# Kernel tuning notes

Hardware: AMD Instinct MI355X
Metric: run time of the kernel (lower is better)

The kernel has to match this reference:

```python
import jax, jax.numpy as jnp
import numpy as np


def setup_inputs() -> dict:
    key = jax.random.key(0)
    k1, k2 = jax.random.split(key)
    B, S, K, N = 8, 2048, 2048, 2048
    a = jax.random.normal(k1, (B, S, K), dtype=jnp.float32)
    b = jax.random.normal(k2, (B, K, N), dtype=jnp.float32)
    return {"a": a, "b": b}


def reference(a, b):
    # Per-sample dense: out[i] = a[i] @ b[i], fused as one batched GEMM.
    # a: [B, S, K], b: [B, K, N] -> out: [B, S, N]
    return jnp.einsum('bsk,bkn->bsn', a, b)
```

## Files before the change

### kernel.cpp

```cpp
#include <hip/hip_runtime.h>

#define BATCH 8
#define SDIM 2048
#define KDIM 2048
#define NDIM 2048

typedef __bf16 bf16_t;
typedef bf16_t bf16x4 __attribute__((ext_vector_type(4)));
typedef bf16_t bf16x8 __attribute__((ext_vector_type(8)));
typedef float f32x4 __attribute__((ext_vector_type(4)));
typedef float f32x8 __attribute__((ext_vector_type(8)));
typedef unsigned short u16x8 __attribute__((ext_vector_type(8)));

__device__ __forceinline__ void gl_lds16(const void* g, void* l) {
    __builtin_amdgcn_global_load_lds(
        (__attribute__((address_space(1))) void*)g,
        (__attribute__((address_space(3))) void*)l,
        16, 0, 0);
}

__global__ __launch_bounds__(256)
void cvtA_kernel(const float* __restrict__ A, bf16_t* __restrict__ Abf) {
    const size_t total8 = (size_t)BATCH * SDIM * KDIM / 8;
    const size_t stride = (size_t)gridDim.x * 256;
    for (size_t i = (size_t)blockIdx.x * 256 + threadIdx.x; i < total8; i += stride) {
        f32x8 v = *reinterpret_cast<const f32x8*>(A + i * 8);
        *reinterpret_cast<bf16x8*>(Abf + i * 8) = __builtin_convertvector(v, bf16x8);
    }
}

__global__ __launch_bounds__(256)
void cvtBT_kernel(const float* __restrict__ B, bf16_t* __restrict__ Bt) {
    __shared__ alignas(16) bf16_t T[64][72];
    const int gid = blockIdx.x;
    const int batch = gid & 7;
    const int tile = gid >> 3;
    const int k0g = (tile >> 5) * 64;
    const int n0g = (tile & 31) * 64;
    const float* Bb = B + (size_t)batch * KDIM * NDIM + (size_t)k0g * NDIM + n0g;
    bf16_t* Tb = Bt + (size_t)batch * NDIM * KDIM + (size_t)n0g * KDIM + k0g;

    const int t = threadIdx.x;
    const int kq = t & 15;
    const int nq = t >> 4;
    f32x4 v[4];
#pragma unroll
    for (int r = 0; r < 4; ++r)
        v[r] = *reinterpret_cast<const f32x4*>(Bb + (size_t)(kq * 4 + r) * NDIM + nq * 4);
#pragma unroll
    for (int j = 0; j < 4; ++j) {
        bf16x4 w = {(bf16_t)v[0][j], (bf16_t)v[1][j], (bf16_t)v[2][j], (bf16_t)v[3][j]};
        *reinterpret_cast<bf16x4*>(&T[nq * 4 + j][kq * 4]) = w;
    }
    __syncthreads();
    const int n = t >> 2, kc = t & 3;
    bf16x8 o0 = *reinterpret_cast<const bf16x8*>(&T[n][kc * 16]);
    bf16x8 o1 = *reinterpret_cast<const bf16x8*>(&T[n][kc * 16 + 8]);
    *reinterpret_cast<bf16x8*>(Tb + (size_t)n * KDIM + kc * 16) = o0;
    *reinterpret_cast<bf16x8*>(Tb + (size_t)n * KDIM + kc * 16 + 8) = o1;
}

#define VM4 asm volatile("s_waitcnt vmcnt(4)" ::: "memory")
#define VM0 asm volatile("s_waitcnt vmcnt(0)" ::: "memory")
#define NOOP ((void)0)

__global__ __launch_bounds__(512, 2)
void bgemm_pipe(const bf16_t* __restrict__ A, const bf16_t* __restrict__ Bt,
                float* __restrict__ O) {
    __shared__ alignas(16) bf16_t lds[65536];

    const int tid = threadIdx.x;
    const int gid = blockIdx.x;
    const int batch = gid & 7;
    const int t = gid >> 3;
    const int bm = (t >> 3) * 256;
    const int bn = (t & 7) * 256;

    const int lane = tid & 63;
    const int wid = tid >> 6;
    const int wr = wid >> 2;
    const int wc = wid & 3;
    const int lr = lane & 15;
    const int lq = lane >> 4;

    const bf16_t* Ab = A + (size_t)batch * SDIM * KDIM;
    const bf16_t* Bb = Bt + (size_t)batch * NDIM * KDIM;
    float* Ob = O + (size_t)batch * SDIM * NDIM;

    const bf16_t* aSrc0 = Ab + (size_t)(bm + wid * 32 + lr) * KDIM + lq * 8;
    const bf16_t* aSrc1 = aSrc0 + (size_t)16 * KDIM;
    const bf16_t* bSrc0 = Bb + (size_t)(bn + wid * 32 + lr) * KDIM + lq * 8;
    const bf16_t* bSrc1 = bSrc0 + (size_t)16 * KDIM;

    const int aDst0 = (wid * 2) * 512;
    const int aDst1 = (wid * 2 + 1) * 512;
    const int rdA = lq * 128 + lr * 8;
    const int rdB = 8192 + lq * 128 + lr * 8;

#define STAGE(BUF_, KT_) do { \
    gl_lds16(aSrc0 + (size_t)(KT_) * 32, &lds[(BUF_) * 16384 + aDst0]); \
    gl_lds16(aSrc1 + (size_t)(KT_) * 32, &lds[(BUF_) * 16384 + aDst1]); \
    gl_lds16(bSrc0 + (size_t)(KT_) * 32, &lds[(BUF_) * 16384 + 8192 + aDst0]); \
    gl_lds16(bSrc1 + (size_t)(KT_) * 32, &lds[(BUF_) * 16384 + 8192 + aDst1]); \
} while (0)

    f32x4 acc[8][4];
#pragma unroll
    for (int m = 0; m < 8; ++m)
#pragma unroll
        for (int n = 0; n < 4; ++n)
            acc[m][n] = (f32x4){0.f, 0.f, 0.f, 0.f};

    bf16x8 aLo[4], aHi[4], bFr[4];

#define READ_LOB(BUF_) do { \
    _Pragma("unroll") \
    for (int m_ = 0; m_ < 4; ++m_) \
        aLo[m_] = *reinterpret_cast<const bf16x8*>( \
            &lds[(BUF_) * 16384 + (wr * 8 + m_) * 512 + rdA]); \
    _Pragma("unroll") \
    for (int n_ = 0; n_ < 4; ++n_) \
        bFr[n_] = *reinterpret_cast<const bf16x8*>( \
            &lds[(BUF_) * 16384 + (wc * 4 + n_) * 512 + rdB]); \
} while (0)

#define READ_HI(BUF_) do { \
    _Pragma("unroll") \
    for (int m_ = 0; m_ < 4; ++m_) \
        aHi[m_] = *reinterpret_cast<const bf16x8*>( \
            &lds[(BUF_) * 16384 + (wr * 8 + 4 + m_) * 512 + rdA]); \
} while (0)

#define MFMA_LO do { \
    __builtin_amdgcn_s_setprio(1); \
    _Pragma("unroll") \
    for (int m_ = 0; m_ < 4; ++m_) \
        _Pragma("unroll") \
        for (int n_ = 0; n_ < 4; ++n_) \
            acc[m_][n_] = __builtin_amdgcn_mfma_f32_16x16x32_bf16( \
                aLo[m_], bFr[n_], acc[m_][n_], 0, 0, 0); \
    __builtin_amdgcn_s_setprio(0); \
} while (0)

#define MFMA_HI do { \
    __builtin_amdgcn_s_setprio(1); \
    _Pragma("unroll") \
    for (int m_ = 0; m_ < 4; ++m_) \
        _Pragma("unroll") \
        for (int n_ = 0; n_ < 4; ++n_) \
            acc[4 + m_][n_] = __builtin_amdgcn_mfma_f32_16x16x32_bf16( \
                aHi[m_], bFr[n_], acc[4 + m_][n_], 0, 0, 0); \
    __builtin_amdgcn_s_setprio(0); \
} while (0)

#define BODY(BUF_, J_, DO_HI_, DO_STAGE_, VM_STMT, DO_BAR_) do { \
    if (DO_HI_) MFMA_HI; \
    READ_LOB(BUF_); \
    if (DO_STAGE_) STAGE(((J_) + 2) & 3, (J_) + 2); \
    READ_HI(BUF_); \
    MFMA_LO; \
    VM_STMT; \
    if (DO_BAR_) __builtin_amdgcn_s_barrier(); \
} while (0)

    STAGE(0, 0);
    STAGE(1, 1);
    VM4;
    __builtin_amdgcn_s_barrier();

    BODY(0, 0, 0, 1, VM4, 1);

#pragma unroll 1
    for (int j4 = 1; j4 < 61; j4 += 4) {
        BODY(1, j4 + 0, 1, 1, VM4, 1);
        BODY(2, j4 + 1, 1, 1, VM4, 1);
        BODY(3, j4 + 2, 1, 1, VM4, 1);
        BODY(0, j4 + 3, 1, 1, VM4, 1);
    }
    BODY(1, 61, 1, 1, VM4, 1);
    BODY(2, 62, 1, 0, VM0, 1);
    BODY(3, 63, 1, 0, NOOP, 0);
    MFMA_HI;

#pragma unroll
    for (int m = 0; m < 8; ++m) {
        const int row0 = bm + wr * 128 + m * 16 + lq * 4;
#pragma unroll
        for (int n = 0; n < 4; ++n) {
            const int col = bn + wc * 64 + n * 16 + lr;
#pragma unroll
            for (int j = 0; j < 4; ++j)
                Ob[(size_t)(row0 + j) * NDIM + col] = acc[m][n][j];
        }
    }
#undef BODY
#undef MFMA_HI
#undef MFMA_LO
#undef READ_HI
#undef READ_LOB
#undef STAGE
}

__device__ __forceinline__ unsigned short f2bf(float f) {
    unsigned int u = __builtin_bit_cast(unsigned int, f);
    u += 0x7fffu + ((u >> 16) & 1u);
    return (unsigned short)(u >> 16);
}

__global__ __launch_bounds__(256, 2)
void bgemm_fused(const float* __restrict__ A, const float* __restrict__ B,
                 float* __restrict__ O) {
    __shared__ alignas(16) unsigned short Asl[2][4 * 128 * 8];
    __shared__ alignas(16) unsigned short Bsl[2][4 * 128 * 8];
    const int tid = threadIdx.x;
    const int gid = blockIdx.x;
    const int batch = gid & 7;
    const int t = gid >> 3;
    const int bm = (t >> 4) * 128;
    const int bn = (t & 15) * 128;
    const float* Ab = A + (size_t)batch * SDIM * KDIM;
    const float* Bb = B + (size_t)batch * KDIM * NDIM;
    float* Ob = O + (size_t)batch * SDIM * NDIM;
    const int lane = tid & 63;
    const int wid = tid >> 6;
    const int wr = wid >> 1, wc = wid & 1;
    const int lr = lane & 15, lq = lane >> 4;
    const int r0 = tid & 127, h0 = tid >> 7;
    u16x8 areg[2], breg[2];
    f32x4 acc[4][4];
#pragma unroll
    for (int m = 0; m < 4; ++m)
#pragma unroll
        for (int n = 0; n < 4; ++n) acc[m][n] = (f32x4){0.f, 0.f, 0.f, 0.f};
    auto stage_regs = [&](int kt) {
        const int k0 = kt * 32;
        const float* ap = Ab + (size_t)(bm + r0) * KDIM + k0 + h0 * 16;
        float4 a0 = *reinterpret_cast<const float4*>(ap + 0);
        float4 a1 = *reinterpret_cast<const float4*>(ap + 4);
        float4 a2 = *reinterpret_cast<const float4*>(ap + 8);
        float4 a3 = *reinterpret_cast<const float4*>(ap + 12);
        u16x8 u;
        u[0]=f2bf(a0.x);u[1]=f2bf(a0.y);u[2]=f2bf(a0.z);u[3]=f2bf(a0.w);
        u[4]=f2bf(a1.x);u[5]=f2bf(a1.y);u[6]=f2bf(a1.z);u[7]=f2bf(a1.w);
        areg[0]=u;
        u[0]=f2bf(a2.x);u[1]=f2bf(a2.y);u[2]=f2bf(a2.z);u[3]=f2bf(a2.w);
        u[4]=f2bf(a3.x);u[5]=f2bf(a3.y);u[6]=f2bf(a3.z);u[7]=f2bf(a3.w);
        areg[1]=u;
        const float* bp = Bb + (size_t)(k0 + h0 * 16) * NDIM + bn + r0;
        float f[16];
#pragma unroll
        for (int j = 0; j < 16; ++j) f[j] = bp[(size_t)j * NDIM];
        u16x8 v;
#pragma unroll
        for (int j = 0; j < 8; ++j) v[j] = f2bf(f[j]);
        breg[0] = v;
#pragma unroll
        for (int j = 0; j < 8; ++j) v[j] = f2bf(f[8 + j]);
        breg[1] = v;
    };
    auto regs_to_lds = [&](int b) {
#pragma unroll
        for (int o = 0; o < 2; ++o) {
            *reinterpret_cast<u16x8*>(&Asl[b][((h0*2+o)*128 + r0)*8]) = areg[o];
            *reinterpret_cast<u16x8*>(&Bsl[b][((h0*2+o)*128 + r0)*8]) = breg[o];
        }
    };
    stage_regs(0);
    regs_to_lds(0);
    int buf = 0;
    for (int kt = 0; kt < KDIM / 32; ++kt) {
        if (kt + 1 < KDIM / 32) stage_regs(kt + 1);
        __syncthreads();
        bf16x8 af[4], bfv[4];
#pragma unroll
        for (int m = 0; m < 4; ++m)
            af[m] = *reinterpret_cast<const bf16x8*>(&Asl[buf][(lq*128 + wr*64 + m*16 + lr)*8]);
#pragma unroll
        for (int n = 0; n < 4; ++n)
            bfv[n] = *reinterpret_cast<const bf16x8*>(&Bsl[buf][(lq*128 + wc*64 + n*16 + lr)*8]);
#pragma unroll
        for (int m = 0; m < 4; ++m)
#pragma unroll
            for (int n = 0; n < 4; ++n)
                acc[m][n] = __builtin_amdgcn_mfma_f32_16x16x32_bf16(af[m], bfv[n], acc[m][n], 0, 0, 0);
        if (kt + 1 < KDIM / 32) regs_to_lds(buf ^ 1);
        buf ^= 1;
    }
#pragma unroll
    for (int m = 0; m < 4; ++m) {
        const int row0 = bm + wr * 64 + m * 16 + lq * 4;
#pragma unroll
        for (int n = 0; n < 4; ++n) {
            const int col = bn + wc * 64 + n * 16 + lr;
#pragma unroll
            for (int j = 0; j < 4; ++j)
                Ob[(size_t)(row0 + j) * NDIM + col] = acc[m][n][j];
        }
    }
}

extern "C" void kernel_launch(void* const* d_in, const int* in_sizes, int n_in,
                              void* d_out, int out_size, void* d_ws, size_t ws_size,
                              hipStream_t stream) {
    const float* a = (const float*)d_in[0];
    const float* b = (const float*)d_in[1];
    float* o = (float*)d_out;
    const size_t half = (size_t)BATCH * SDIM * KDIM * sizeof(bf16_t);
    if (ws_size >= 2 * half) {
        bf16_t* Abf = (bf16_t*)d_ws;
        bf16_t* Bt = (bf16_t*)((char*)d_ws + half);
        hipLaunchKernelGGL(cvtA_kernel, dim3(4096), dim3(256), 0, stream, a, Abf);
        hipLaunchKernelGGL(cvtBT_kernel, dim3(8192), dim3(256), 0, stream, b, Bt);
        hipLaunchKernelGGL(bgemm_pipe, dim3(512), dim3(512), 0, stream, Abf, Bt, o);
    } else {
        hipLaunchKernelGGL(bgemm_fused, dim3(2048), dim3(256), 0, stream, a, b, o);
    }
}
```

Baseline: 251.5 us.

## Double-buffer LDS fragment reads in registers to overlap with MFMA

Restructures the GEMM main loop so the A-low and B fragments for the next k-tile are read from LDS into a second register set while MFMAs run on the current set. The prologue and epilogue are reworked to match, and a sched_barrier pins the instruction order. This aims to hide LDS read latency behind matrix-core work. In exchange it needs many more fragment registers alongside a large accumulator, so with two 512-thread blocks per CU it risks register spills or lower occupancy.

```diff
diff --git a/kernel.cpp b/kernel.cpp
--- a/kernel.cpp
+++ b/kernel.cpp
@@ -62,10 +62,11 @@
 
 #define VM4 asm volatile("s_waitcnt vmcnt(4)" ::: "memory")
 #define VM0 asm volatile("s_waitcnt vmcnt(0)" ::: "memory")
-#define NOOP ((void)0)
+#define BAR __builtin_amdgcn_s_barrier()
+#define SCHED __builtin_amdgcn_sched_barrier(0)
 
 __global__ __launch_bounds__(512, 2)
-void bgemm_pipe(const bf16_t* __restrict__ A, const bf16_t* __restrict__ Bt,
+void bgemm_dbuf(const bf16_t* __restrict__ A, const bf16_t* __restrict__ Bt,
                 float* __restrict__ O) {
     __shared__ alignas(16) bf16_t lds[65536];
 
@@ -111,76 +112,88 @@
         for (int n = 0; n < 4; ++n)
             acc[m][n] = (f32x4){0.f, 0.f, 0.f, 0.f};
 
-    bf16x8 aLo[4], aHi[4], bFr[4];
-
-#define READ_LOB(BUF_) do { \
+    bf16x8 aLo0[4], aLo1[4], bF0[4], bF1[4], aHi[4];
+
+#define READ_NXT(P_, RBOFF_) do { \
     _Pragma("unroll") \
     for (int m_ = 0; m_ < 4; ++m_) \
-        aLo[m_] = *reinterpret_cast<const bf16x8*>( \
-            &lds[(BUF_) * 16384 + (wr * 8 + m_) * 512 + rdA]); \
+        aLo##P_[m_] = *reinterpret_cast<const bf16x8*>( \
+            &lds[(RBOFF_) + (wr * 8 + m_) * 512 + rdA]); \
     _Pragma("unroll") \
     for (int n_ = 0; n_ < 4; ++n_) \
-        bFr[n_] = *reinterpret_cast<const bf16x8*>( \
-            &lds[(BUF_) * 16384 + (wc * 4 + n_) * 512 + rdB]); \
-} while (0)
-
-#define READ_HI(BUF_) do { \
+        bF##P_[n_] = *reinterpret_cast<const bf16x8*>( \
+            &lds[(RBOFF_) + (wc * 4 + n_) * 512 + rdB]); \
+} while (0)
+
+#define READ_HI(RBOFF_) do { \
     _Pragma("unroll") \
     for (int m_ = 0; m_ < 4; ++m_) \
         aHi[m_] = *reinterpret_cast<const bf16x8*>( \
-            &lds[(BUF_) * 16384 + (wr * 8 + 4 + m_) * 512 + rdA]); \
-} while (0)
-
-#define MFMA_LO do { \
+            &lds[(RBOFF_) + (wr * 8 + 4 + m_) * 512 + rdA]); \
+} while (0)
+
+#define MFMA_LO(P_) do { \
     __builtin_amdgcn_s_setprio(1); \
     _Pragma("unroll") \
     for (int m_ = 0; m_ < 4; ++m_) \
         _Pragma("unroll") \
         for (int n_ = 0; n_ < 4; ++n_) \
             acc[m_][n_] = __builtin_amdgcn_mfma_f32_16x16x32_bf16( \
-                aLo[m_], bFr[n_], acc[m_][n_], 0, 0, 0); \
+                aLo##P_[m_], bF##P_[n_], acc[m_][n_], 0, 0, 0); \
     __builtin_amdgcn_s_setprio(0); \
 } while (0)
 
-#define MFMA_HI do { \
+#define MFMA_HI(P_) do { \
     __builtin_amdgcn_s_setprio(1); \
     _Pragma("unroll") \
     for (int m_ = 0; m_ < 4; ++m_) \
         _Pragma("unroll") \
         for (int n_ = 0; n_ < 4; ++n_) \
             acc[4 + m_][n_] = __builtin_amdgcn_mfma_f32_16x16x32_bf16( \
-                aHi[m_], bFr[n_], acc[4 + m_][n_], 0, 0, 0); \
+                aHi[m_], bF##P_[n_], acc[4 + m_][n_], 0, 0, 0); \
     __builtin_amdgcn_s_setprio(0); \
 } while (0)
 
-#define BODY(BUF_, J_, DO_HI_, DO_STAGE_, VM_STMT, DO_BAR_) do { \
-    if (DO_HI_) MFMA_HI; \
-    READ_LOB(BUF_); \
-    if (DO_STAGE_) STAGE(((J_) + 2) & 3, (J_) + 2); \
-    READ_HI(BUF_); \
-    MFMA_LO; \
-    VM_STMT; \
-    if (DO_BAR_) __builtin_amdgcn_s_barrier(); \
+#define BODY(CUR_, NXT_, RB_, SB_, KT_) do { \
+    READ_NXT(NXT_, (RB_) * 16384); \
+    STAGE(SB_, KT_); \
+    SCHED; \
+    MFMA_LO(CUR_); \
+    MFMA_HI(CUR_); \
+    READ_HI((RB_) * 16384); \
+    VM4; \
+    BAR; \
 } while (0)
 
     STAGE(0, 0);
     STAGE(1, 1);
     VM4;
-    __builtin_amdgcn_s_barrier();
-
-    BODY(0, 0, 0, 1, VM4, 1);
+    BAR;
+    STAGE(2, 2);
+    READ_NXT(0, 0);
+    READ_HI(0);
+    VM4;
+    BAR;
 
 #pragma unroll 1
-    for (int j4 = 1; j4 < 61; j4 += 4) {
-        BODY(1, j4 + 0, 1, 1, VM4, 1);
-        BODY(2, j4 + 1, 1, 1, VM4, 1);
-        BODY(3, j4 + 2, 1, 1, VM4, 1);
-        BODY(0, j4 + 3, 1, 1, VM4, 1);
-    }
-    BODY(1, 61, 1, 1, VM4, 1);
-    BODY(2, 62, 1, 0, VM0, 1);
-    BODY(3, 63, 1, 0, NOOP, 0);
-    MFMA_HI;
+    for (int j4 = 0; j4 < 60; j4 += 4) {
+        BODY(0, 1, 1, 3, j4 + 3);
+        BODY(1, 0, 2, 0, j4 + 4);
+        BODY(0, 1, 3, 1, j4 + 5);
+        BODY(1, 0, 0, 2, j4 + 6);
+    }
+    BODY(0, 1, 1, 3, 63);
+    READ_NXT(0, 2 * 16384);
+    SCHED;
+    MFMA_LO(1); MFMA_HI(1);
+    READ_HI(2 * 16384);
+    VM0;
+    BAR;
+    READ_NXT(1, 3 * 16384);
+    SCHED;
+    MFMA_LO(0); MFMA_HI(0);
+    READ_HI(3 * 16384);
+    MFMA_LO(1); MFMA_HI(1);
 
 #pragma unroll
     for (int m = 0; m < 8; ++m) {
@@ -197,7 +210,7 @@
 #undef MFMA_HI
 #undef MFMA_LO
 #undef READ_HI
-#undef READ_LOB
+#undef READ_NXT
 #undef STAGE
 }
 
@@ -311,7 +324,7 @@
         bf16_t* Bt = (bf16_t*)((char*)d_ws + half);
         hipLaunchKernelGGL(cvtA_kernel, dim3(4096), dim3(256), 0, stream, a, Abf);
         hipLaunchKernelGGL(cvtBT_kernel, dim3(8192), dim3(256), 0, stream, b, Bt);
-        hipLaunchKernelGGL(bgemm_pipe, dim3(512), dim3(512), 0, stream, Abf, Bt, o);
+        hipLaunchKernelGGL(bgemm_dbuf, dim3(512), dim3(512), 0, stream, Abf, Bt, o);
     } else {
         hipLaunchKernelGGL(bgemm_fused, dim3(2048), dim3(256), 0, stream, a, b, o);
     }
```

New measurement: 251.8 us. No clear change (+0.1%).
